# Kernel optimization log

Hardware: AMD Instinct MI355X
Metric: run time of the kernel (lower is better)

Reference implementation:

```python
import jax, jax.numpy as jnp
import numpy as np

N_HEADS = 4  # from init_kwargs


def setup_inputs() -> dict:
    rng = jax.random.key(0)
    ks = jax.random.split(rng, 7)
    S, B, D = 512, 16, 2048  # seqlen must equal head_dim (D // N_HEADS) per module's reshape
    w_scale = 0.02  # keep logits in a sane range so softmax is not one-hot
    return {
        "query": jax.random.normal(ks[0], (S, B, D), dtype=jnp.float32),
        "key": jax.random.normal(ks[1], (S, B, D), dtype=jnp.float32),
        "value": jax.random.normal(ks[2], (S, B, D), dtype=jnp.float32),
        "Wq": jax.random.normal(ks[3], (D, D), dtype=jnp.float32) * w_scale,
        "Wk": jax.random.normal(ks[4], (D, D), dtype=jnp.float32) * w_scale,
        "Wv": jax.random.normal(ks[5], (D, D), dtype=jnp.float32) * w_scale,
        "Wo": jax.random.normal(ks[6], (D, D), dtype=jnp.float32) * w_scale,
    }


def reference(query, key, value, Wq, Wk, Wv, Wo):
    # Dropout layers act as identity (inference mode). RoPE helper exists in the
    # original module but is never invoked in forward(), so it is omitted.
    S, B, D = query.shape
    H = N_HEADS
    hd = D // H  # head_dim; note S == hd is required by the original reshapes

    def split_heads(x, W):
        # torch Linear: x @ W.T ; then (S,B,D)->(S,B,H,hd)->(H,B,S,hd)->(H*B,S,hd)
        y = x @ W.T
        return y.reshape(S, B, H, hd).transpose(2, 1, 0, 3).reshape(H * B, S, hd)

    q = split_heads(query, Wq)
    k = split_heads(key, Wk)
    v = split_heads(value, Wv)

    scores = jnp.einsum("nsd,ntd->nst", q, k) / jnp.sqrt(jnp.float32(hd))
    attn = jax.nn.softmax(scores, axis=-1)          # (H*B, S, S)
    out = jnp.einsum("nst,ntd->nsd", attn, v)        # (H*B, S, hd)

    # output: (H*B,S,hd)->(H,B,S,hd)->permute(1,2,0,3)->(B,S,H,hd)
    out4 = out.reshape(H, B, S, hd).transpose(1, 2, 0, 3)
    # attn_score reshape relies on S == hd, faithfully reproduced
    attn_score = attn.reshape(H, B, S, hd).transpose(1, 2, 0, 3)  # (B,S,H,hd)

    # .transpose(1,2).contiguous().view(S,B,-1): row-major reinterpret of (B,H,S,hd)
    out4 = jnp.swapaxes(out4, 1, 2)  # (B,H,S,hd)
    output = out4.reshape(S, B, D)

    output = output @ Wo.T
    return output, attn_score
```

## Files before the change

kernel.cpp:

```cpp
#include <hip/hip_runtime.h>
#include <hip/hip_bf16.h>
#include <math.h>

using bf16 = __hip_bfloat16;
typedef __attribute__((ext_vector_type(4))) float f32x4;
typedef __attribute__((ext_vector_type(8))) short s16x8;

#define BM 256
#define BN 256
#define BK 32
#define SLOT 16384
#define BREG 8192

__device__ __forceinline__ short f2b(float f) {
  bf16 h = __float2bfloat16(f);
  short s; __builtin_memcpy(&s, &h, 2); return s;
}

__device__ __forceinline__ void async16(const bf16* g, bf16* l) {
  __builtin_amdgcn_global_load_lds(
      (const __attribute__((address_space(1))) void*)g,
      (__attribute__((address_space(3))) void*)l, 16, 0, 0);
}

template<int MODE, bool CF32>
__global__ __launch_bounds__(512, 2) void gemm_nt(const bf16* __restrict__ Ain,
    const bf16* __restrict__ Bin, void* __restrict__ Cout,
    int K, int lda, int ldb, int ldc, float alpha)
{
  __shared__ bf16 lds[4 * SLOT];

  const int tid  = threadIdx.x;
  const int lane = tid & 63;
  const int wave = tid >> 6;
  const int quad = lane >> 4;
  const int l16  = lane & 15;

  const int nwg = gridDim.x * gridDim.y * gridDim.z;
  int bid = (blockIdx.z * gridDim.y + blockIdx.y) * gridDim.x + blockIdx.x;
  bid = (bid & 7) * (nwg >> 3) + (bid >> 3);
  const int bx = bid % gridDim.x;
  int rest = bid / gridDim.x;
  const int by = rest % gridDim.y;
  const int bz = rest / gridDim.y;

  size_t aBase = 0, bBase = 0, cBase = 0;
  if (MODE == 1) {
    aBase = (size_t)bz * 262144;
    bBase = (size_t)bz * 262144;
    cBase = (size_t)(bz & 15) * 1048576 + (size_t)(bz >> 4) * 512;
  } else if (MODE == 2) {
    aBase = (size_t)(bz & 15) * 1048576 + (size_t)(bz >> 4) * 512;
    bBase = (size_t)bz * 262144;
    cBase = (size_t)((bz & 15) * 4 + (bz >> 4)) * 262144;
  }

  const int tileM = by * BM;
  const int tileN = bx * BN;

  const int sRow = tid >> 2;
  const int sQ   = (tid & 3) ^ ((tid >> 3) & 3);
  const int sCol = sQ * 8;
  const size_t aOff0 = aBase + (size_t)(tileM + sRow) * lda + sCol;
  const size_t aOff1 = aOff0 + (size_t)128 * lda;
  const size_t bOff0 = bBase + (size_t)(tileN + sRow) * ldb + sCol;
  const size_t bOff1 = bOff0 + (size_t)128 * ldb;
  const int t8 = tid * 8;

  const int warpRow = (wave >> 2) * 128;
  const int warpCol = (wave & 3) * 64;
  int offA[8], offB[4];
#pragma unroll
  for (int mi = 0; mi < 8; mi++) {
    const int R = warpRow + mi * 16 + l16;
    offA[mi] = R * 32 + ((quad ^ ((R >> 1) & 3)) * 8);
  }
#pragma unroll
  for (int ni = 0; ni < 4; ni++) {
    const int R = warpCol + ni * 16 + l16;
    offB[ni] = BREG + R * 32 + ((quad ^ ((R >> 1) & 3)) * 8);
  }

  f32x4 acc[8][4] = {};
  const int NT = K / BK;

#pragma unroll
  for (int p = 0; p < 3; ++p) {
    bf16* base = lds + p * SLOT;
    const int ks = p * BK;
    async16(Ain + aOff0 + ks, base + t8);
    async16(Ain + aOff1 + ks, base + 4096 + t8);
    async16(Bin + bOff0 + ks, base + BREG + t8);
    async16(Bin + bOff1 + ks, base + BREG + 4096 + t8);
  }
  asm volatile("s_waitcnt vmcnt(8)" ::: "memory");
  __builtin_amdgcn_s_barrier();

  for (int g = 0; g < NT; ++g) {
    if (g + 3 < NT) {
      bf16* base = lds + ((g + 3) & 3) * SLOT;
      const int ks = (g + 3) * BK;
      async16(Ain + aOff0 + ks, base + t8);
      async16(Ain + aOff1 + ks, base + 4096 + t8);
      async16(Bin + bOff0 + ks, base + BREG + t8);
      async16(Bin + bOff1 + ks, base + BREG + 4096 + t8);
    }

    const bf16* lb = lds + (g & 3) * SLOT;
    s16x8 af[8], bfr[4];
#pragma unroll
    for (int mi = 0; mi < 8; mi++) af[mi] = *(const s16x8*)(lb + offA[mi]);
#pragma unroll
    for (int ni = 0; ni < 4; ni++) bfr[ni] = *(const s16x8*)(lb + offB[ni]);

    __builtin_amdgcn_s_setprio(1);
#pragma unroll
    for (int mi = 0; mi < 8; mi++)
#pragma unroll
      for (int ni = 0; ni < 4; ni++)
        acc[mi][ni] = __builtin_amdgcn_mfma_f32_16x16x32_bf16(af[mi], bfr[ni], acc[mi][ni], 0, 0, 0);
    __builtin_amdgcn_s_setprio(0);

    if (g < NT - 1) {
      const int ahead = (g + 3 < NT ? 2 : (g + 2 < NT ? NT - 2 - g : 0));
      if (ahead == 2)      asm volatile("s_waitcnt vmcnt(8)" ::: "memory");
      else if (ahead == 1) asm volatile("s_waitcnt vmcnt(4)" ::: "memory");
      else                 asm volatile("s_waitcnt vmcnt(0)" ::: "memory");
      __builtin_amdgcn_s_barrier();
    }
  }

#pragma unroll
  for (int mi = 0; mi < 8; mi++) {
#pragma unroll
    for (int ni = 0; ni < 4; ni++) {
      f32x4 v = acc[mi][ni];
      const int col = tileN + warpCol + ni * 16 + l16;
#pragma unroll
      for (int r = 0; r < 4; r++) {
        const int row = tileM + warpRow + mi * 16 + quad * 4 + r;
        const float val = v[r] * alpha;
        size_t dst;
        if (MODE == 0) {
          dst = (((size_t)((col >> 9) * 16 + (row & 15)) * 512 + (size_t)(row >> 4)) * 512)
                + (size_t)(col & 511);
        } else {
          dst = cBase + (size_t)row * ldc + (size_t)col;
        }
        if (CF32) ((float*)Cout)[dst] = val;
        else      ((bf16*)Cout)[dst] = __float2bfloat16(val);
      }
    }
  }
}

struct Conv6 {
  const float* src[6];
  bf16* dst[6];
  int n[6];
};

__global__ __launch_bounds__(256) void convert6(Conv6 a) {
  const int t = blockIdx.y;
  const float* __restrict__ src = a.src[t];
  bf16* __restrict__ dst = a.dst[t];
  const size_t n = (size_t)a.n[t];
  const size_t stride = (size_t)gridDim.x * 2048;
  for (size_t i = ((size_t)blockIdx.x * 256 + threadIdx.x) * 8; i < n; i += stride) {
    f32x4 x = *(const f32x4*)(src + i);
    f32x4 y = *(const f32x4*)(src + i + 4);
    s16x8 r;
    r[0] = f2b(x[0]); r[1] = f2b(x[1]); r[2] = f2b(x[2]); r[3] = f2b(x[3]);
    r[4] = f2b(y[0]); r[5] = f2b(y[1]); r[6] = f2b(y[2]); r[7] = f2b(y[3]);
    *(s16x8*)(dst + i) = r;
  }
}

__global__ __launch_bounds__(256) void softmax512f(float* __restrict__ P,
                                                   bf16* __restrict__ Pb) {
  const int row  = blockIdx.x * 4 + (threadIdx.x >> 6);
  const int lane = threadIdx.x & 63;
  float* p = P + (size_t)row * 512 + lane * 8;
  bf16* pb = Pb + (size_t)row * 512 + lane * 8;

  f32x4 a = *(const f32x4*)p;
  f32x4 b = *(const f32x4*)(p + 4);
  float v[8];
  float m = -1e30f;
#pragma unroll
  for (int j = 0; j < 4; j++) { v[j] = a[j]; v[j + 4] = b[j]; }
#pragma unroll
  for (int j = 0; j < 8; j++) m = fmaxf(m, v[j]);
#pragma unroll
  for (int off = 32; off > 0; off >>= 1) m = fmaxf(m, __shfl_xor(m, off, 64));
  float s = 0.f;
#pragma unroll
  for (int j = 0; j < 8; j++) { v[j] = __expf(v[j] - m); s += v[j]; }
#pragma unroll
  for (int off = 32; off > 0; off >>= 1) s += __shfl_xor(s, off, 64);
  const float inv = 1.f / s;
  f32x4 oa, ob;
  s16x8 rb;
#pragma unroll
  for (int j = 0; j < 4; j++) { oa[j] = v[j] * inv; ob[j] = v[j + 4] * inv; }
#pragma unroll
  for (int j = 0; j < 8; j++) rb[j] = f2b(v[j] * inv);
  *(f32x4*)p = oa;
  *(f32x4*)(p + 4) = ob;
  *(s16x8*)pb = rb;
}

__global__ __launch_bounds__(256) void transpose512(const bf16* __restrict__ V,
                                                    bf16* __restrict__ VT) {
  __shared__ bf16 tile[32][33];
  const int n = blockIdx.z;
  const bf16* src = V + (size_t)n * 262144;
  bf16* dst = VT + (size_t)n * 262144;
  const int x = blockIdx.x * 32 + threadIdx.x;
#pragma unroll
  for (int i = 0; i < 32; i += 8)
    tile[threadIdx.y + i][threadIdx.x] =
        src[(size_t)(blockIdx.y * 32 + threadIdx.y + i) * 512 + x];
  __syncthreads();
  const int tcol = blockIdx.y * 32 + threadIdx.x;
#pragma unroll
  for (int i = 0; i < 32; i += 8)
    dst[(size_t)(blockIdx.x * 32 + threadIdx.y + i) * 512 + tcol] =
        tile[threadIdx.x][threadIdx.y + i];
}

extern "C" void kernel_launch(void* const* d_in, const int* in_sizes, int n_in,
                              void* d_out, int out_size, void* d_ws, size_t ws_size,
                              hipStream_t stream) {
  const float* query = (const float*)d_in[0];
  const float* key   = (const float*)d_in[1];
  const float* value = (const float*)d_in[2];
  const float* Wq = (const float*)d_in[3];
  const float* Wk = (const float*)d_in[4];
  const float* Wv = (const float*)d_in[5];
  const float* Wo = (const float*)d_in[6];
  float* out = (float*)d_out;
  float* P   = out + 16777216;

  bf16* ws0 = (bf16*)d_ws;
  bf16* ws1 = ws0 + 16777216;
  bf16* o0  = (bf16*)d_out;
  bf16* o1  = o0 + 16777216;
  bf16* p0  = (bf16*)P;
  bf16* p1  = p0 + 16777216;

  const dim3 blk(256);
  const dim3 gblk(512);
  const float inv_sqrt_hd = 0.04419417382415922f;

  Conv6 c;
  c.src[0] = query; c.dst[0] = ws0;           c.n[0] = 16777216;
  c.src[1] = key;   c.dst[1] = ws1;           c.n[1] = 16777216;
  c.src[2] = value; c.dst[2] = p0;            c.n[2] = 16777216;
  c.src[3] = Wq;    c.dst[3] = p1;            c.n[3] = 4194304;
  c.src[4] = Wk;    c.dst[4] = p1 + 4194304;  c.n[4] = 4194304;
  c.src[5] = Wv;    c.dst[5] = p1 + 8388608;  c.n[5] = 4194304;
  convert6<<<dim3(2048, 6), blk, 0, stream>>>(c);

  gemm_nt<0, false><<<dim3(8, 32, 1), gblk, 0, stream>>>(ws0, p1,           o0,  2048, 2048, 2048, 0, 1.0f);
  gemm_nt<0, false><<<dim3(8, 32, 1), gblk, 0, stream>>>(ws1, p1 + 4194304, o1,  2048, 2048, 2048, 0, 1.0f);
  gemm_nt<0, false><<<dim3(8, 32, 1), gblk, 0, stream>>>(p0,  p1 + 8388608, ws0, 2048, 2048, 2048, 0, 1.0f);

  transpose512<<<dim3(16, 16, 64), dim3(32, 8), 0, stream>>>(ws0, ws1);

  gemm_nt<1, true><<<dim3(2, 2, 64), gblk, 0, stream>>>(o0, o1, P, 512, 512, 512, 2048, inv_sqrt_hd);

  softmax512f<<<dim3(8192), blk, 0, stream>>>(P, o0);

  gemm_nt<2, false><<<dim3(2, 2, 64), gblk, 0, stream>>>(o0, ws1, ws0, 512, 2048, 512, 512, 1.0f);

  Conv6 cw;
  for (int i = 0; i < 6; i++) { cw.src[i] = Wo; cw.dst[i] = ws1; cw.n[i] = 4194304; }
  convert6<<<dim3(2048, 1), blk, 0, stream>>>(cw);

  gemm_nt<3, true><<<dim3(8, 32, 1), gblk, 0, stream>>>(ws0, ws1, out, 2048, 2048, 2048, 2048, 1.0f);
}
```

Measured before the change: 698.1 us.

## Fuse QK^T scores GEMM with row softmax and widen convert kernel

```diff
diff --git a/kernel.cpp b/kernel.cpp
--- a/kernel.cpp
+++ b/kernel.cpp
@@ -21,6 +21,13 @@
   __builtin_amdgcn_global_load_lds(
       (const __attribute__((address_space(1))) void*)g,
       (__attribute__((address_space(3))) void*)l, 16, 0, 0);
+}
+
+__device__ __forceinline__ f32x4 vmax4(f32x4 a, f32x4 b) {
+  f32x4 r;
+#pragma unroll
+  for (int j = 0; j < 4; j++) r[j] = fmaxf(a[j], b[j]);
+  return r;
 }
 
 template<int MODE, bool CF32>
@@ -45,11 +52,7 @@
   const int bz = rest / gridDim.y;
 
   size_t aBase = 0, bBase = 0, cBase = 0;
-  if (MODE == 1) {
-    aBase = (size_t)bz * 262144;
-    bBase = (size_t)bz * 262144;
-    cBase = (size_t)(bz & 15) * 1048576 + (size_t)(bz >> 4) * 512;
-  } else if (MODE == 2) {
+  if (MODE == 2) {
     aBase = (size_t)(bz & 15) * 1048576 + (size_t)(bz >> 4) * 512;
     bBase = (size_t)bz * 262144;
     cBase = (size_t)((bz & 15) * 4 + (bz >> 4)) * 262144;
@@ -154,6 +157,189 @@
   }
 }
 
+#define SSLOT 20480
+__global__ __launch_bounds__(512, 2) void scores_softmax(
+    const bf16* __restrict__ Q, const bf16* __restrict__ Kh,
+    float* __restrict__ P, bf16* __restrict__ Pb, float alpha)
+{
+  __shared__ bf16 lds[3 * SSLOT];
+
+  const int tid  = threadIdx.x;
+  const int lane = tid & 63;
+  const int wave = tid >> 6;
+  const int quad = lane >> 4;
+  const int l16  = lane & 15;
+
+  int bid = blockIdx.z * 4 + blockIdx.y;
+  bid = (bid & 7) * 32 + (bid >> 3);
+  const int by = bid & 3;
+  const int bz = bid >> 2;
+
+  const size_t aBase = (size_t)bz * 262144;
+  const size_t bBase = (size_t)bz * 262144;
+  const size_t cBase = (size_t)(bz & 15) * 1048576 + (size_t)(bz >> 4) * 512;
+  const int tileM = by * 128;
+
+  const int sRow = tid >> 2;
+  const int sQz  = (tid & 3) ^ ((tid >> 3) & 3);
+  const int sCol = sQz * 8;
+  const size_t aOff = aBase + (size_t)(tileM + sRow) * 512 + sCol;
+  const size_t bOff = bBase + (size_t)sRow * 512 + sCol;
+  const int t8 = tid * 8;
+
+  const int warpRow = (wave >> 2) * 64;
+  const int warpCol = (wave & 3) * 128;
+  int offA[4], offB[8];
+#pragma unroll
+  for (int mi = 0; mi < 4; mi++) {
+    const int R = warpRow + mi * 16 + l16;
+    offA[mi] = R * 32 + ((quad ^ ((R >> 1) & 3)) * 8);
+  }
+#pragma unroll
+  for (int ni = 0; ni < 8; ni++) {
+    const int R = warpCol + ni * 16 + l16;
+    offB[ni] = 4096 + R * 32 + ((quad ^ ((R >> 1) & 3)) * 8);
+  }
+
+  f32x4 acc[4][8] = {};
+
+#pragma unroll
+  for (int p = 0; p < 2; ++p) {
+    bf16* base = lds + p * SSLOT;
+    const int ks = p * BK;
+    async16(Q + aOff + ks, base + t8);
+#pragma unroll
+    for (int c = 0; c < 4; c++)
+      async16(Kh + bOff + c * 65536 + ks, base + 4096 + c * 4096 + t8);
+  }
+  asm volatile("s_waitcnt vmcnt(5)" ::: "memory");
+  __builtin_amdgcn_s_barrier();
+
+  for (int g = 0; g < 16; ++g) {
+    if (g + 2 < 16) {
+      bf16* base = lds + ((g + 2) % 3) * SSLOT;
+      const int ks = (g + 2) * BK;
+      async16(Q + aOff + ks, base + t8);
+#pragma unroll
+      for (int c = 0; c < 4; c++)
+        async16(Kh + bOff + c * 65536 + ks, base + 4096 + c * 4096 + t8);
+    }
+
+    const bf16* lb = lds + (g % 3) * SSLOT;
+    s16x8 af[4], bfr[8];
+#pragma unroll
+    for (int mi = 0; mi < 4; mi++) af[mi] = *(const s16x8*)(lb + offA[mi]);
+#pragma unroll
+    for (int ni = 0; ni < 8; ni++) bfr[ni] = *(const s16x8*)(lb + offB[ni]);
+
+    __builtin_amdgcn_s_setprio(1);
+#pragma unroll
+    for (int mi = 0; mi < 4; mi++)
+#pragma unroll
+      for (int ni = 0; ni < 8; ni++)
+        acc[mi][ni] = __builtin_amdgcn_mfma_f32_16x16x32_bf16(af[mi], bfr[ni], acc[mi][ni], 0, 0, 0);
+    __builtin_amdgcn_s_setprio(0);
+
+    if (g + 2 < 16) {
+      asm volatile("s_waitcnt vmcnt(5)" ::: "memory");
+      __builtin_amdgcn_s_barrier();
+    } else if (g + 1 < 16) {
+      asm volatile("s_waitcnt vmcnt(0)" ::: "memory");
+      __builtin_amdgcn_s_barrier();
+    }
+  }
+
+  __syncthreads();
+  float* red  = (float*)lds;
+  float* red2 = red + 512;
+  const int wv = wave & 3;
+
+#pragma unroll
+  for (int mi = 0; mi < 4; mi++)
+#pragma unroll
+    for (int ni = 0; ni < 8; ni++) acc[mi][ni] *= alpha;
+
+  f32x4 gm[4];
+#pragma unroll
+  for (int mi = 0; mi < 4; mi++) {
+    f32x4 mx = acc[mi][0];
+#pragma unroll
+    for (int ni = 1; ni < 8; ni++) mx = vmax4(mx, acc[mi][ni]);
+#pragma unroll
+    for (int off = 1; off <= 8; off <<= 1) {
+      f32x4 o;
+#pragma unroll
+      for (int r = 0; r < 4; r++) o[r] = __shfl_xor(mx[r], off, 64);
+      mx = vmax4(mx, o);
+    }
+    if (l16 == 0) {
+      const int rw = warpRow + mi * 16 + quad * 4;
+#pragma unroll
+      for (int r = 0; r < 4; r++) red[(rw + r) * 4 + wv] = mx[r];
+    }
+  }
+  __syncthreads();
+#pragma unroll
+  for (int mi = 0; mi < 4; mi++) {
+    const int rw = warpRow + mi * 16 + quad * 4;
+#pragma unroll
+    for (int r = 0; r < 4; r++) {
+      f32x4 p = *(const f32x4*)&red[(rw + r) * 4];
+      gm[mi][r] = fmaxf(fmaxf(p[0], p[1]), fmaxf(p[2], p[3]));
+    }
+  }
+  f32x4 sm[4] = {};
+#pragma unroll
+  for (int mi = 0; mi < 4; mi++)
+#pragma unroll
+    for (int ni = 0; ni < 8; ni++) {
+      f32x4 v = acc[mi][ni];
+#pragma unroll
+      for (int r = 0; r < 4; r++) v[r] = __expf(v[r] - gm[mi][r]);
+      acc[mi][ni] = v;
+      sm[mi] += v;
+    }
+#pragma unroll
+  for (int mi = 0; mi < 4; mi++) {
+#pragma unroll
+    for (int off = 1; off <= 8; off <<= 1) {
+      f32x4 o;
+#pragma unroll
+      for (int r = 0; r < 4; r++) o[r] = __shfl_xor(sm[mi][r], off, 64);
+      sm[mi] += o;
+    }
+    if (l16 == 0) {
+      const int rw = warpRow + mi * 16 + quad * 4;
+#pragma unroll
+      for (int r = 0; r < 4; r++) red2[(rw + r) * 4 + wv] = sm[mi][r];
+    }
+  }
+  __syncthreads();
+#pragma unroll
+  for (int mi = 0; mi < 4; mi++) {
+    const int rw = warpRow + mi * 16 + quad * 4;
+#pragma unroll
+    for (int r = 0; r < 4; r++) {
+      f32x4 p = *(const f32x4*)&red2[(rw + r) * 4];
+      gm[mi][r] = 1.f / (p[0] + p[1] + p[2] + p[3]);
+    }
+  }
+#pragma unroll
+  for (int mi = 0; mi < 4; mi++)
+#pragma unroll
+    for (int ni = 0; ni < 8; ni++) {
+      const int col = warpCol + ni * 16 + l16;
+#pragma unroll
+      for (int r = 0; r < 4; r++) {
+        const int row = tileM + warpRow + mi * 16 + quad * 4 + r;
+        const size_t idx = cBase + (size_t)row * 2048 + col;
+        const float val = acc[mi][ni][r] * gm[mi][r];
+        P[idx]  = val;
+        Pb[idx] = __float2bfloat16(val);
+      }
+    }
+}
+
 struct Conv6 {
   const float* src[6];
   bf16* dst[6];
@@ -165,49 +351,23 @@
   const float* __restrict__ src = a.src[t];
   bf16* __restrict__ dst = a.dst[t];
   const size_t n = (size_t)a.n[t];
-  const size_t stride = (size_t)gridDim.x * 2048;
-  for (size_t i = ((size_t)blockIdx.x * 256 + threadIdx.x) * 8; i < n; i += stride) {
-    f32x4 x = *(const f32x4*)(src + i);
-    f32x4 y = *(const f32x4*)(src + i + 4);
-    s16x8 r;
-    r[0] = f2b(x[0]); r[1] = f2b(x[1]); r[2] = f2b(x[2]); r[3] = f2b(x[3]);
-    r[4] = f2b(y[0]); r[5] = f2b(y[1]); r[6] = f2b(y[2]); r[7] = f2b(y[3]);
-    *(s16x8*)(dst + i) = r;
-  }
-}
-
-__global__ __launch_bounds__(256) void softmax512f(float* __restrict__ P,
-                                                   bf16* __restrict__ Pb) {
-  const int row  = blockIdx.x * 4 + (threadIdx.x >> 6);
-  const int lane = threadIdx.x & 63;
-  float* p = P + (size_t)row * 512 + lane * 8;
-  bf16* pb = Pb + (size_t)row * 512 + lane * 8;
-
-  f32x4 a = *(const f32x4*)p;
-  f32x4 b = *(const f32x4*)(p + 4);
-  float v[8];
-  float m = -1e30f;
-#pragma unroll
-  for (int j = 0; j < 4; j++) { v[j] = a[j]; v[j + 4] = b[j]; }
-#pragma unroll
-  for (int j = 0; j < 8; j++) m = fmaxf(m, v[j]);
-#pragma unroll
-  for (int off = 32; off > 0; off >>= 1) m = fmaxf(m, __shfl_xor(m, off, 64));
-  float s = 0.f;
-#pragma unroll
-  for (int j = 0; j < 8; j++) { v[j] = __expf(v[j] - m); s += v[j]; }
-#pragma unroll
-  for (int off = 32; off > 0; off >>= 1) s += __shfl_xor(s, off, 64);
-  const float inv = 1.f / s;
-  f32x4 oa, ob;
-  s16x8 rb;
-#pragma unroll
-  for (int j = 0; j < 4; j++) { oa[j] = v[j] * inv; ob[j] = v[j + 4] * inv; }
-#pragma unroll
-  for (int j = 0; j < 8; j++) rb[j] = f2b(v[j] * inv);
-  *(f32x4*)p = oa;
-  *(f32x4*)(p + 4) = ob;
-  *(s16x8*)pb = rb;
+  const size_t stride = (size_t)gridDim.x * 256 * 64;
+  for (size_t i = ((size_t)blockIdx.x * 256 + threadIdx.x) * 64; i < n; i += stride) {
+    f32x4 x[16];
+#pragma unroll
+    for (int j = 0; j < 16; j++) x[j] = *(const f32x4*)(src + i + j * 4);
+    s16x8 r[8];
+#pragma unroll
+    for (int j = 0; j < 8; j++) {
+#pragma unroll
+      for (int k = 0; k < 4; k++) {
+        r[j][k]     = f2b(x[2 * j][k]);
+        r[j][4 + k] = f2b(x[2 * j + 1][k]);
+      }
+    }
+#pragma unroll
+    for (int j = 0; j < 8; j++) *(s16x8*)(dst + i + j * 8) = r[j];
+  }
 }
 
 __global__ __launch_bounds__(256) void transpose512(const bf16* __restrict__ V,
@@ -260,23 +420,21 @@
   c.src[3] = Wq;    c.dst[3] = p1;            c.n[3] = 4194304;
   c.src[4] = Wk;    c.dst[4] = p1 + 4194304;  c.n[4] = 4194304;
   c.src[5] = Wv;    c.dst[5] = p1 + 8388608;  c.n[5] = 4194304;
-  convert6<<<dim3(2048, 6), blk, 0, stream>>>(c);
+  convert6<<<dim3(1024, 6), blk, 0, stream>>>(c);
 
   gemm_nt<0, false><<<dim3(8, 32, 1), gblk, 0, stream>>>(ws0, p1,           o0,  2048, 2048, 2048, 0, 1.0f);
   gemm_nt<0, false><<<dim3(8, 32, 1), gblk, 0, stream>>>(ws1, p1 + 4194304, o1,  2048, 2048, 2048, 0, 1.0f);
   gemm_nt<0, false><<<dim3(8, 32, 1), gblk, 0, stream>>>(p0,  p1 + 8388608, ws0, 2048, 2048, 2048, 0, 1.0f);
 
-  transpose512<<<dim3(16, 16, 64), dim3(32, 8), 0, stream>>>(ws0, ws1);
-
-  gemm_nt<1, true><<<dim3(2, 2, 64), gblk, 0, stream>>>(o0, o1, P, 512, 512, 512, 2048, inv_sqrt_hd);
-
-  softmax512f<<<dim3(8192), blk, 0, stream>>>(P, o0);
-
-  gemm_nt<2, false><<<dim3(2, 2, 64), gblk, 0, stream>>>(o0, ws1, ws0, 512, 2048, 512, 512, 1.0f);
+  scores_softmax<<<dim3(1, 4, 64), gblk, 0, stream>>>(o0, o1, P, ws1, inv_sqrt_hd);
+
+  transpose512<<<dim3(16, 16, 64), dim3(32, 8), 0, stream>>>(ws0, o0);
+
+  gemm_nt<2, false><<<dim3(2, 2, 64), gblk, 0, stream>>>(ws1, o0, ws0, 512, 2048, 512, 512, 1.0f);
 
   Conv6 cw;
   for (int i = 0; i < 6; i++) { cw.src[i] = Wo; cw.dst[i] = ws1; cw.n[i] = 4194304; }
-  convert6<<<dim3(2048, 1), blk, 0, stream>>>(cw);
+  convert6<<<dim3(256, 1), blk, 0, stream>>>(cw);
 
   gemm_nt<3, true><<<dim3(8, 32, 1), gblk, 0, stream>>>(ws0, ws1, out, 2048, 2048, 2048, 2048, 1.0f);
 }
```

Measured after the change: 711.0 us. No clear change (+1.8%).
